# Kernel optimization log

Measured on AMD Instinct MI355X. Metric: run time of the kernel, lower is better.

The kernel has to match this reference:

```python
import jax, jax.numpy as jnp
import numpy as np

N_NODES = 50000
N_EDGES = 800000
D = 128
N_LAYERS = 5  # 1 input + 3 hidden + 1 output MaxAggConv layers


def setup_inputs() -> dict:
    key = jax.random.key(0)
    k1, k2, k3, k4 = jax.random.split(key, 4)
    x = jax.random.normal(k1, (N_NODES, D), dtype=jnp.float32)
    edge_index = jax.random.randint(k2, (2, N_EDGES), 0, N_NODES, dtype=jnp.int64)
    # Linear params per layer (all layers are D->D here): W [out,in], b [out]
    Ws = jax.random.normal(k3, (N_LAYERS, D, D), dtype=jnp.float32) * (1.0 / np.sqrt(D))
    bs = jax.random.normal(k4, (N_LAYERS, D), dtype=jnp.float32) * 0.01
    return {"x": x, "edge_index": edge_index, "Ws": Ws, "bs": bs}


def _max_agg_conv(x, src, dst, W, b, n_nodes):
    # Linear: x @ W^T + b  (nn.Linear convention)
    h = jnp.einsum('nd,od->no', x, W) + b
    # gather per-edge messages x_j (source nodes), scatter-max into targets
    m = jax.ops.segment_max(h[src], dst, num_segments=n_nodes)
    # PyG scatter-max fills nodes with no incoming edges with 0
    return jnp.where(jnp.isneginf(m), 0.0, m)


def reference(x, edge_index, Ws, bs):
    src = edge_index[0]
    dst = edge_index[1]
    n = x.shape[0]
    for i in range(N_LAYERS - 1):
        x = _max_agg_conv(x, src, dst, Ws[i], bs[i], n)
        x = jax.nn.silu(x)
    x = _max_agg_conv(x, src, dst, Ws[N_LAYERS - 1], bs[N_LAYERS - 1], n)
    return x
```

## Files before the change

### kernel.cpp

```cpp
#include <hip/hip_runtime.h>
#include <hip/hip_bf16.h>
#include <hip/hip_fp16.h>
#include <math.h>

#define DF 128
#define NLAYERS 5

typedef __attribute__((ext_vector_type(8))) _Float16 f16x8;
typedef __attribute__((ext_vector_type(4))) _Float16 f16x4;
typedef __attribute__((ext_vector_type(4))) float f32x4;

__device__ inline unsigned pkmax(unsigned a, unsigned b) {
    unsigned d;
    asm("v_pk_max_f16 %0, %1, %2" : "=v"(d) : "v"(a), "v"(b));
    return d;
}
__device__ inline float h2f(unsigned short u) {
    __half_raw r; r.x = u;
    return __half2float(__half(r));
}
__device__ inline float silu(float v) {
    return v * (1.0f / (1.0f + __expf(-v)));
}

__device__ inline void split8f(const float* p, f16x8& hi, f16x8& lo) {
    float4 v0 = *reinterpret_cast<const float4*>(p);
    float4 v1 = *reinterpret_cast<const float4*>(p + 4);
    float f[8] = {v0.x, v0.y, v0.z, v0.w, v1.x, v1.y, v1.z, v1.w};
#pragma unroll
    for (int j = 0; j < 8; ++j) {
        _Float16 a = (_Float16)f[j];
        hi[j] = a;
        lo[j] = (_Float16)(f[j] - (float)a);
    }
}


__global__ __launch_bounds__(256) void zero_kernel(int* __restrict__ p, int n) {
    int i = blockIdx.x * 256 + threadIdx.x;
    if (i < n) p[i] = 0;
}


__global__ __launch_bounds__(256) void prep_kernel(const int* __restrict__ dst,
        int* __restrict__ cnt, unsigned short* __restrict__ rank, int E, int nbE,
        const float* __restrict__ Ws, _Float16* __restrict__ whf,
        _Float16* __restrict__ wlf, int wt4) {
    int b = blockIdx.x;
    int t = threadIdx.x;
    if (b < nbE) {
        int i = b * 256 + t;
        if (i < E) rank[i] = (unsigned short)atomicAdd(&cnt[dst[i]], 1);
    } else {
        int i = (b - nbE) * 256 + t;
        if (i < wt4) {
            float4 v = reinterpret_cast<const float4*>(Ws)[i];
            float f[4] = {v.x, v.y, v.z, v.w};
            f16x4 h, l;
#pragma unroll
            for (int j = 0; j < 4; ++j) {
                _Float16 a = (_Float16)f[j];
                h[j] = a;
                l[j] = (_Float16)(f[j] - (float)a);
            }
            reinterpret_cast<f16x4*>(whf)[i] = h;
            reinterpret_cast<f16x4*>(wlf)[i] = l;
        }
    }
}


__global__ __launch_bounds__(256) void partial_sum_kernel(const int* __restrict__ cnt,
        int* __restrict__ bsum, int n) {
    __shared__ int red[256];
    int t = threadIdx.x;
    int i = blockIdx.x * 256 + t;
    red[t] = (i < n) ? cnt[i] : 0;
    __syncthreads();
    for (int d = 128; d > 0; d >>= 1) {
        if (t < d) red[t] += red[t + d];
        __syncthreads();
    }
    if (t == 0) bsum[blockIdx.x] = red[0];
}

__global__ __launch_bounds__(256) void scan_scatter_kernel(const int* __restrict__ cnt,
        const int* __restrict__ bsum, int* __restrict__ off, int n, int E, int nb) {
    __shared__ int sb[256];
    __shared__ int s[256];
    int t = threadIdx.x;
    int bv = (t < nb) ? bsum[t] : 0;
    sb[t] = bv;
    __syncthreads();
    for (int d = 1; d < 256; d <<= 1) {
        int u = (t >= d) ? sb[t - d] : 0;
        __syncthreads();
        sb[t] += u;
        __syncthreads();
    }
    int base = (blockIdx.x > 0) ? sb[blockIdx.x - 1] : 0;
    int i = blockIdx.x * 256 + t;
    int v = (i < n) ? cnt[i] : 0;
    s[t] = v;
    __syncthreads();
    for (int d = 1; d < 256; d <<= 1) {
        int u = (t >= d) ? s[t - d] : 0;
        __syncthreads();
        s[t] += u;
        __syncthreads();
    }
    int excl = s[t] - v + base;
    if (i < n) off[i] = excl;
    if (blockIdx.x == 0 && t == 0) off[n] = E;
}


__global__ __launch_bounds__(256, 3) void fill_gemm0_kernel(
        const int* __restrict__ src, const int* __restrict__ dst,
        const int* __restrict__ off, const unsigned short* __restrict__ rank,
        unsigned short* __restrict__ csr, int E, int nbE,
        const float* __restrict__ x,
        const _Float16* __restrict__ whf, const _Float16* __restrict__ wlf,
        const float* __restrict__ bias, __half* __restrict__ h, int n) {
    if (blockIdx.x < nbE) {
        int i = blockIdx.x * 256 + threadIdx.x;
        if (i < E) csr[off[dst[i]] + (int)rank[i]] = (unsigned short)src[i];
        return;
    }
    int bid = blockIdx.x - nbE;

    int wave = threadIdx.x >> 6;
    int lane = threadIdx.x & 63;
    int wm = wave >> 1;
    int wn = wave & 1;
    int m0 = bid * 64 + wm * 32;
    int n0 = wn * 64;
    int lr = lane & 15;
    int lk = lane >> 4;

    f32x4 acc[2][4];
#pragma unroll
    for (int mt = 0; mt < 2; ++mt)
#pragma unroll
        for (int nt = 0; nt < 4; ++nt) {
            float bv = bias[n0 + nt * 16 + lr];
            acc[mt][nt] = (f32x4){bv, bv, bv, bv};
        }

    int rowA0 = min(m0 + lr, n - 1);
    int rowA1 = min(m0 + 16 + lr, n - 1);

#pragma unroll
    for (int ks = 0; ks < 4; ++ks) {
        int ko = ks * 32 + lk * 8;
        f16x8 a0h, a0l, a1h, a1l;
        split8f(x + (size_t)rowA0 * DF + ko, a0h, a0l);
        split8f(x + (size_t)rowA1 * DF + ko, a1h, a1l);
#pragma unroll
        for (int nt = 0; nt < 4; ++nt) {
            int ncol = n0 + nt * 16 + lr;
            f16x8 wh = *(const f16x8*)(whf + ncol * DF + ko);
            f16x8 wl = *(const f16x8*)(wlf + ncol * DF + ko);
            acc[0][nt] = __builtin_amdgcn_mfma_f32_16x16x32_f16(a0h, wh, acc[0][nt], 0, 0, 0);
            acc[0][nt] = __builtin_amdgcn_mfma_f32_16x16x32_f16(a0l, wh, acc[0][nt], 0, 0, 0);
            acc[0][nt] = __builtin_amdgcn_mfma_f32_16x16x32_f16(a0h, wl, acc[0][nt], 0, 0, 0);
            acc[1][nt] = __builtin_amdgcn_mfma_f32_16x16x32_f16(a1h, wh, acc[1][nt], 0, 0, 0);
            acc[1][nt] = __builtin_amdgcn_mfma_f32_16x16x32_f16(a1l, wh, acc[1][nt], 0, 0, 0);
            acc[1][nt] = __builtin_amdgcn_mfma_f32_16x16x32_f16(a1h, wl, acc[1][nt], 0, 0, 0);
        }
    }

#pragma unroll
    for (int mt = 0; mt < 2; ++mt) {
        int rbase = m0 + mt * 16 + lk * 4;
#pragma unroll
        for (int j = 0; j < 4; ++j) {
            int r = rbase + j;
            if (r < n) {
#pragma unroll
                for (int nt = 0; nt < 4; ++nt)
                    h[(size_t)r * DF + n0 + nt * 16 + lr] = __float2half(acc[mt][nt][j]);
            }
        }
    }
}


__global__ __launch_bounds__(256, 3) void gemm_f16_kernel(
        const _Float16* __restrict__ xf,
        const _Float16* __restrict__ whf, const _Float16* __restrict__ wlf,
        const float* __restrict__ bias, __half* __restrict__ h, int n) {
    int wave = threadIdx.x >> 6;
    int lane = threadIdx.x & 63;
    int wm = wave >> 1;
    int wn = wave & 1;
    int m0 = blockIdx.x * 64 + wm * 32;
    int n0 = wn * 64;
    int lr = lane & 15;
    int lk = lane >> 4;

    f32x4 acc[2][4];
#pragma unroll
    for (int mt = 0; mt < 2; ++mt)
#pragma unroll
        for (int nt = 0; nt < 4; ++nt) {
            float bv = bias[n0 + nt * 16 + lr];
            acc[mt][nt] = (f32x4){bv, bv, bv, bv};
        }

    int rowA0 = min(m0 + lr, n - 1);
    int rowA1 = min(m0 + 16 + lr, n - 1);

#pragma unroll
    for (int ks = 0; ks < 4; ++ks) {
        int ko = ks * 32 + lk * 8;
        f16x8 a0 = *(const f16x8*)(xf + (size_t)rowA0 * DF + ko);
        f16x8 a1 = *(const f16x8*)(xf + (size_t)rowA1 * DF + ko);
#pragma unroll
        for (int nt = 0; nt < 4; ++nt) {
            int ncol = n0 + nt * 16 + lr;
            f16x8 wh = *(const f16x8*)(whf + ncol * DF + ko);
            f16x8 wl = *(const f16x8*)(wlf + ncol * DF + ko);
            acc[0][nt] = __builtin_amdgcn_mfma_f32_16x16x32_f16(a0, wh, acc[0][nt], 0, 0, 0);
            acc[0][nt] = __builtin_amdgcn_mfma_f32_16x16x32_f16(a0, wl, acc[0][nt], 0, 0, 0);
            acc[1][nt] = __builtin_amdgcn_mfma_f32_16x16x32_f16(a1, wh, acc[1][nt], 0, 0, 0);
            acc[1][nt] = __builtin_amdgcn_mfma_f32_16x16x32_f16(a1, wl, acc[1][nt], 0, 0, 0);
        }
    }

#pragma unroll
    for (int mt = 0; mt < 2; ++mt) {
        int rbase = m0 + mt * 16 + lk * 4;
#pragma unroll
        for (int j = 0; j < 4; ++j) {
            int r = rbase + j;
            if (r < n) {
#pragma unroll
                for (int nt = 0; nt < 4; ++nt)
                    h[(size_t)r * DF + n0 + nt * 16 + lr] = __float2half(acc[mt][nt][j]);
            }
        }
    }
}


__global__ __launch_bounds__(256) void agg_kernel(const __half* __restrict__ hin,
        const int* __restrict__ off, const unsigned short* __restrict__ csr,
        float* __restrict__ out, _Float16* __restrict__ xf, int n, int split) {
    int wid = threadIdx.x >> 6;
    int lane = threadIdx.x & 63;
    int node = blockIdx.x * 4 + wid;
    if (node >= n) return;

    int hf = lane >> 5;
    int l = lane & 31;
    const uint2* h2 = (const uint2*)hin;

    int beg = off[node];
    int end = off[node + 1];

    unsigned m0 = 0xFC00FC00u;
    unsigned m1 = 0xFC00FC00u;

    int e1 = end - 1;
    for (int k = beg; k < end; k += 16) {
        int k0 = k + hf;
        int i0 = min(k0,      e1), i1 = min(k0 + 2,  e1);
        int i2 = min(k0 + 4,  e1), i3 = min(k0 + 6,  e1);
        int i4 = min(k0 + 8,  e1), i5 = min(k0 + 10, e1);
        int i6 = min(k0 + 12, e1), i7 = min(k0 + 14, e1);
        int s0 = csr[i0], s1 = csr[i1], s2 = csr[i2], s3 = csr[i3];
        int s4 = csr[i4], s5 = csr[i5], s6 = csr[i6], s7 = csr[i7];
        uint2 a0 = h2[s0 * 32 + l];
        uint2 a1 = h2[s1 * 32 + l];
        uint2 a2 = h2[s2 * 32 + l];
        uint2 a3 = h2[s3 * 32 + l];
        uint2 a4 = h2[s4 * 32 + l];
        uint2 a5 = h2[s5 * 32 + l];
        uint2 a6 = h2[s6 * 32 + l];
        uint2 a7 = h2[s7 * 32 + l];
        m0 = pkmax(m0, pkmax(pkmax(pkmax(a0.x, a1.x), pkmax(a2.x, a3.x)),
                             pkmax(pkmax(a4.x, a5.x), pkmax(a6.x, a7.x))));
        m1 = pkmax(m1, pkmax(pkmax(pkmax(a0.y, a1.y), pkmax(a2.y, a3.y)),
                             pkmax(pkmax(a4.y, a5.y), pkmax(a6.y, a7.y))));
    }

    m0 = pkmax(m0, (unsigned)__shfl_xor((int)m0, 32));
    m1 = pkmax(m1, (unsigned)__shfl_xor((int)m1, 32));

    if (hf != 0) return;

    float f0 = h2f((unsigned short)(m0 & 0xFFFF));
    float f1 = h2f((unsigned short)(m0 >> 16));
    float f2 = h2f((unsigned short)(m1 & 0xFFFF));
    float f3 = h2f((unsigned short)(m1 >> 16));
    if (beg == end) { f0 = f1 = f2 = f3 = 0.0f; }

    if (split) {
        f0 = silu(f0); f1 = silu(f1); f2 = silu(f2); f3 = silu(f3);
        f16x4 v = { (_Float16)f0, (_Float16)f1, (_Float16)f2, (_Float16)f3 };
        *reinterpret_cast<f16x4*>(xf + (size_t)node * DF + l * 4) = v;
    } else {
        float4 v = make_float4(f0, f1, f2, f3);
        reinterpret_cast<float4*>(out)[node * 32 + l] = v;
    }
}


extern "C" void kernel_launch(void* const* d_in, const int* in_sizes, int n_in,
                              void* d_out, int out_size, void* d_ws, size_t ws_size,
                              hipStream_t stream) {
    const float* x  = (const float*)d_in[0];
    const int*   ei = (const int*)d_in[1];
    const float* Ws = (const float*)d_in[2];
    const float* bs = (const float*)d_in[3];
    float* out = (float*)d_out;

    int N = in_sizes[0] / DF;
    int E = in_sizes[1] / 2;
    const int* src = ei;
    const int* dst = ei + E;

    char* w = (char*)d_ws;
    auto carve = [&](size_t bytes) {
        char* p = w;
        w += (bytes + 255) & ~(size_t)255;
        return p;
    };
    int nb = (N + 255) / 256;
    int*            cnt  = (int*)carve((size_t)(N + 1) * sizeof(int));
    int*            off  = (int*)carve((size_t)(N + 1) * sizeof(int));
    int*            bsum = (int*)carve((size_t)nb * sizeof(int));
    unsigned short* rank = (unsigned short*)carve((size_t)E * sizeof(unsigned short));
    unsigned short* csr  = (unsigned short*)carve((size_t)E * sizeof(unsigned short));
    __half*         h    = (__half*)carve((size_t)N * DF * sizeof(__half));
    _Float16*       xf   = (_Float16*)carve((size_t)N * DF * sizeof(_Float16));
    _Float16*       whf  = (_Float16*)carve((size_t)NLAYERS * DF * DF * sizeof(_Float16));
    _Float16*       wlf  = (_Float16*)carve((size_t)NLAYERS * DF * DF * sizeof(_Float16));

    int nbE = (E + 255) / 256;
    int wt4 = NLAYERS * DF * DF / 4;
    int nbW = (wt4 + 255) / 256;
    int ggrid = (N + 63) / 64;
    int agrid = (N + 3) / 4;

    zero_kernel<<<nb, 256, 0, stream>>>(cnt, N);
    prep_kernel<<<nbE + nbW, 256, 0, stream>>>(dst, cnt, rank, E, nbE, Ws, whf, wlf, wt4);
    partial_sum_kernel<<<nb, 256, 0, stream>>>(cnt, bsum, N);
    scan_scatter_kernel<<<nb, 256, 0, stream>>>(cnt, bsum, off, N, E, nb);

    fill_gemm0_kernel<<<nbE + ggrid, 256, 0, stream>>>(
        src, dst, off, rank, csr, E, nbE, x, whf, wlf, bs, h, N);

    for (int layer = 1; layer < NLAYERS; ++layer) {
        agg_kernel<<<agrid, 256, 0, stream>>>(h, off, csr, out, xf, N, 1);
        const _Float16* whl = whf + (size_t)layer * DF * DF;
        const _Float16* wll = wlf + (size_t)layer * DF * DF;
        const float* bl = bs + (size_t)layer * DF;
        gemm_f16_kernel<<<ggrid, 256, 0, stream>>>(xf, whl, wll, bl, h, N);
    }
    agg_kernel<<<agrid, 256, 0, stream>>>(h, off, csr, out, NULL, N, 0);
}
```

Before: 332.3 us.

## Fuse max-aggregation and SiLU with next layer GEMM via LDS staging

Each hidden layer now runs in one 1024-thread kernel. The kernel gathers neighbour max values for 64 nodes, applies SiLU, stores the result in swizzled LDS and then runs the MFMA GEMM from LDS. This removes the intermediate xf round trip through global memory and one launch per layer, and uses ping-pong h buffers. The gather also changes to 16-byte loads with four edges in flight per lane, where it previously used 8-byte loads with eight. In exchange, the GEMM must wait at a block barrier for the gather to finish, large blocks can lower occupancy, and less memory-level parallelism per lane could slow the gather.

After: 363.7 us. 1.09x slower.

```diff
diff --git a/kernel.cpp b/kernel.cpp
--- a/kernel.cpp
+++ b/kernel.cpp
@@ -186,124 +186,170 @@
 }
 
 
-__global__ __launch_bounds__(256, 3) void gemm_f16_kernel(
-        const _Float16* __restrict__ xf,
+__global__ __launch_bounds__(1024, 2) void fused_layer_kernel(
+        const __half* __restrict__ hin,
+        const int* __restrict__ off, const unsigned short* __restrict__ csr,
         const _Float16* __restrict__ whf, const _Float16* __restrict__ wlf,
-        const float* __restrict__ bias, __half* __restrict__ h, int n) {
+        const float* __restrict__ bias, __half* __restrict__ hout, int n) {
+    __shared__ __align__(16) char xlds[64 * 256];
+
     int wave = threadIdx.x >> 6;
     int lane = threadIdx.x & 63;
-    int wm = wave >> 1;
-    int wn = wave & 1;
-    int m0 = blockIdx.x * 64 + wm * 32;
-    int n0 = wn * 64;
+    int q = lane >> 4;
+    int c = lane & 15;
+    int nodebase = blockIdx.x * 64;
+
+    if (nodebase + 64 > n) {
+        for (int ofs = threadIdx.x * 16; ofs < 64 * 256; ofs += 1024 * 16)
+            *(uint4*)(xlds + ofs) = make_uint4(0, 0, 0, 0);
+        __syncthreads();
+    }
+
+#pragma unroll
+    for (int i = 0; i < 4; ++i) {
+        int r = wave * 4 + i;
+        int node = nodebase + r;
+        if (node < n) {
+            int beg = off[node];
+            int end = off[node + 1];
+            unsigned m0 = 0xFC00FC00u, m1 = m0, m2 = m0, m3 = m0;
+            if (beg < end) {
+                int e1 = end - 1;
+                for (int k = beg; k < end; k += 16) {
+                    int i0 = min(k + q,      e1), i1 = min(k + q + 4,  e1);
+                    int i2 = min(k + q + 8,  e1), i3 = min(k + q + 12, e1);
+                    int s0 = csr[i0], s1 = csr[i1], s2 = csr[i2], s3 = csr[i3];
+                    uint4 a = *(const uint4*)((const char*)hin + ((size_t)s0 << 8) + (c << 4));
+                    uint4 b = *(const uint4*)((const char*)hin + ((size_t)s1 << 8) + (c << 4));
+                    uint4 d = *(const uint4*)((const char*)hin + ((size_t)s2 << 8) + (c << 4));
+                    uint4 e = *(const uint4*)((const char*)hin + ((size_t)s3 << 8) + (c << 4));
+                    m0 = pkmax(m0, pkmax(pkmax(a.x, b.x), pkmax(d.x, e.x)));
+                    m1 = pkmax(m1, pkmax(pkmax(a.y, b.y), pkmax(d.y, e.y)));
+                    m2 = pkmax(m2, pkmax(pkmax(a.z, b.z), pkmax(d.z, e.z)));
+                    m3 = pkmax(m3, pkmax(pkmax(a.w, b.w), pkmax(d.w, e.w)));
+                }
+                m0 = pkmax(m0, (unsigned)__shfl_xor((int)m0, 16));
+                m0 = pkmax(m0, (unsigned)__shfl_xor((int)m0, 32));
+                m1 = pkmax(m1, (unsigned)__shfl_xor((int)m1, 16));
+                m1 = pkmax(m1, (unsigned)__shfl_xor((int)m1, 32));
+                m2 = pkmax(m2, (unsigned)__shfl_xor((int)m2, 16));
+                m2 = pkmax(m2, (unsigned)__shfl_xor((int)m2, 32));
+                m3 = pkmax(m3, (unsigned)__shfl_xor((int)m3, 16));
+                m3 = pkmax(m3, (unsigned)__shfl_xor((int)m3, 32));
+            }
+            if (q == 0) {
+                float f[8];
+                f[0] = h2f((unsigned short)(m0 & 0xFFFF)); f[1] = h2f((unsigned short)(m0 >> 16));
+                f[2] = h2f((unsigned short)(m1 & 0xFFFF)); f[3] = h2f((unsigned short)(m1 >> 16));
+                f[4] = h2f((unsigned short)(m2 & 0xFFFF)); f[5] = h2f((unsigned short)(m2 >> 16));
+                f[6] = h2f((unsigned short)(m3 & 0xFFFF)); f[7] = h2f((unsigned short)(m3 >> 16));
+                f16x8 v;
+#pragma unroll
+                for (int j = 0; j < 8; ++j) {
+                    float t = (beg == end) ? 0.0f : silu(f[j]);
+                    v[j] = (_Float16)t;
+                }
+                int bc = (c << 4) ^ ((r & 7) << 4);
+                *(f16x8*)(xlds + r * 256 + bc) = v;
+            }
+        }
+    }
+    __syncthreads();
+
+    int rt = (wave & 3) * 16;
+    int n0 = (wave >> 2) * 32;
     int lr = lane & 15;
     int lk = lane >> 4;
 
-    f32x4 acc[2][4];
-#pragma unroll
-    for (int mt = 0; mt < 2; ++mt)
-#pragma unroll
-        for (int nt = 0; nt < 4; ++nt) {
-            float bv = bias[n0 + nt * 16 + lr];
-            acc[mt][nt] = (f32x4){bv, bv, bv, bv};
-        }
-
-    int rowA0 = min(m0 + lr, n - 1);
-    int rowA1 = min(m0 + 16 + lr, n - 1);
-
+    f32x4 acc[2];
+#pragma unroll
+    for (int nt = 0; nt < 2; ++nt) {
+        float bv = bias[n0 + nt * 16 + lr];
+        acc[nt] = (f32x4){bv, bv, bv, bv};
+    }
+
+    int ar = rt + lr;
 #pragma unroll
     for (int ks = 0; ks < 4; ++ks) {
+        int bo = ks * 64 + lk * 16;
+        f16x8 a = *(const f16x8*)(xlds + ar * 256 + (bo ^ ((ar & 7) << 4)));
         int ko = ks * 32 + lk * 8;
-        f16x8 a0 = *(const f16x8*)(xf + (size_t)rowA0 * DF + ko);
-        f16x8 a1 = *(const f16x8*)(xf + (size_t)rowA1 * DF + ko);
-#pragma unroll
-        for (int nt = 0; nt < 4; ++nt) {
+#pragma unroll
+        for (int nt = 0; nt < 2; ++nt) {
             int ncol = n0 + nt * 16 + lr;
             f16x8 wh = *(const f16x8*)(whf + ncol * DF + ko);
             f16x8 wl = *(const f16x8*)(wlf + ncol * DF + ko);
-            acc[0][nt] = __builtin_amdgcn_mfma_f32_16x16x32_f16(a0, wh, acc[0][nt], 0, 0, 0);
-            acc[0][nt] = __builtin_amdgcn_mfma_f32_16x16x32_f16(a0, wl, acc[0][nt], 0, 0, 0);
-            acc[1][nt] = __builtin_amdgcn_mfma_f32_16x16x32_f16(a1, wh, acc[1][nt], 0, 0, 0);
-            acc[1][nt] = __builtin_amdgcn_mfma_f32_16x16x32_f16(a1, wl, acc[1][nt], 0, 0, 0);
-        }
-    }
-
-#pragma unroll
-    for (int mt = 0; mt < 2; ++mt) {
-        int rbase = m0 + mt * 16 + lk * 4;
-#pragma unroll
-        for (int j = 0; j < 4; ++j) {
-            int r = rbase + j;
-            if (r < n) {
-#pragma unroll
-                for (int nt = 0; nt < 4; ++nt)
-                    h[(size_t)r * DF + n0 + nt * 16 + lr] = __float2half(acc[mt][nt][j]);
-            }
-        }
-    }
-}
-
-
-__global__ __launch_bounds__(256) void agg_kernel(const __half* __restrict__ hin,
+            acc[nt] = __builtin_amdgcn_mfma_f32_16x16x32_f16(a, wh, acc[nt], 0, 0, 0);
+            acc[nt] = __builtin_amdgcn_mfma_f32_16x16x32_f16(a, wl, acc[nt], 0, 0, 0);
+        }
+    }
+
+#pragma unroll
+    for (int j = 0; j < 4; ++j) {
+        int row = nodebase + rt + lk * 4 + j;
+        if (row < n) {
+#pragma unroll
+            for (int nt = 0; nt < 2; ++nt)
+                hout[(size_t)row * DF + n0 + nt * 16 + lr] = __float2half(acc[nt][j]);
+        }
+    }
+}
+
+
+__global__ __launch_bounds__(256) void agg_final_kernel(const __half* __restrict__ hin,
         const int* __restrict__ off, const unsigned short* __restrict__ csr,
-        float* __restrict__ out, _Float16* __restrict__ xf, int n, int split) {
+        float* __restrict__ out, int n) {
     int wid = threadIdx.x >> 6;
     int lane = threadIdx.x & 63;
     int node = blockIdx.x * 4 + wid;
     if (node >= n) return;
 
-    int hf = lane >> 5;
-    int l = lane & 31;
-    const uint2* h2 = (const uint2*)hin;
+    int q = lane >> 4;
+    int c = lane & 15;
 
     int beg = off[node];
     int end = off[node + 1];
 
-    unsigned m0 = 0xFC00FC00u;
-    unsigned m1 = 0xFC00FC00u;
-
-    int e1 = end - 1;
-    for (int k = beg; k < end; k += 16) {
-        int k0 = k + hf;
-        int i0 = min(k0,      e1), i1 = min(k0 + 2,  e1);
-        int i2 = min(k0 + 4,  e1), i3 = min(k0 + 6,  e1);
-        int i4 = min(k0 + 8,  e1), i5 = min(k0 + 10, e1);
-        int i6 = min(k0 + 12, e1), i7 = min(k0 + 14, e1);
-        int s0 = csr[i0], s1 = csr[i1], s2 = csr[i2], s3 = csr[i3];
-        int s4 = csr[i4], s5 = csr[i5], s6 = csr[i6], s7 = csr[i7];
-        uint2 a0 = h2[s0 * 32 + l];
-        uint2 a1 = h2[s1 * 32 + l];
-        uint2 a2 = h2[s2 * 32 + l];
-        uint2 a3 = h2[s3 * 32 + l];
-        uint2 a4 = h2[s4 * 32 + l];
-        uint2 a5 = h2[s5 * 32 + l];
-        uint2 a6 = h2[s6 * 32 + l];
-        uint2 a7 = h2[s7 * 32 + l];
-        m0 = pkmax(m0, pkmax(pkmax(pkmax(a0.x, a1.x), pkmax(a2.x, a3.x)),
-                             pkmax(pkmax(a4.x, a5.x), pkmax(a6.x, a7.x))));
-        m1 = pkmax(m1, pkmax(pkmax(pkmax(a0.y, a1.y), pkmax(a2.y, a3.y)),
-                             pkmax(pkmax(a4.y, a5.y), pkmax(a6.y, a7.y))));
-    }
-
-    m0 = pkmax(m0, (unsigned)__shfl_xor((int)m0, 32));
-    m1 = pkmax(m1, (unsigned)__shfl_xor((int)m1, 32));
-
-    if (hf != 0) return;
-
-    float f0 = h2f((unsigned short)(m0 & 0xFFFF));
-    float f1 = h2f((unsigned short)(m0 >> 16));
-    float f2 = h2f((unsigned short)(m1 & 0xFFFF));
-    float f3 = h2f((unsigned short)(m1 >> 16));
-    if (beg == end) { f0 = f1 = f2 = f3 = 0.0f; }
-
-    if (split) {
-        f0 = silu(f0); f1 = silu(f1); f2 = silu(f2); f3 = silu(f3);
-        f16x4 v = { (_Float16)f0, (_Float16)f1, (_Float16)f2, (_Float16)f3 };
-        *reinterpret_cast<f16x4*>(xf + (size_t)node * DF + l * 4) = v;
-    } else {
-        float4 v = make_float4(f0, f1, f2, f3);
-        reinterpret_cast<float4*>(out)[node * 32 + l] = v;
-    }
+    unsigned m0 = 0xFC00FC00u, m1 = m0, m2 = m0, m3 = m0;
+    if (beg < end) {
+        int e1 = end - 1;
+        for (int k = beg; k < end; k += 16) {
+            int i0 = min(k + q,      e1), i1 = min(k + q + 4,  e1);
+            int i2 = min(k + q + 8,  e1), i3 = min(k + q + 12, e1);
+            int s0 = csr[i0], s1 = csr[i1], s2 = csr[i2], s3 = csr[i3];
+            uint4 a = *(const uint4*)((const char*)hin + ((size_t)s0 << 8) + (c << 4));
+            uint4 b = *(const uint4*)((const char*)hin + ((size_t)s1 << 8) + (c << 4));
+            uint4 d = *(const uint4*)((const char*)hin + ((size_t)s2 << 8) + (c << 4));
+            uint4 e = *(const uint4*)((const char*)hin + ((size_t)s3 << 8) + (c << 4));
+            m0 = pkmax(m0, pkmax(pkmax(a.x, b.x), pkmax(d.x, e.x)));
+            m1 = pkmax(m1, pkmax(pkmax(a.y, b.y), pkmax(d.y, e.y)));
+            m2 = pkmax(m2, pkmax(pkmax(a.z, b.z), pkmax(d.z, e.z)));
+            m3 = pkmax(m3, pkmax(pkmax(a.w, b.w), pkmax(d.w, e.w)));
+        }
+        m0 = pkmax(m0, (unsigned)__shfl_xor((int)m0, 16));
+        m0 = pkmax(m0, (unsigned)__shfl_xor((int)m0, 32));
+        m1 = pkmax(m1, (unsigned)__shfl_xor((int)m1, 16));
+        m1 = pkmax(m1, (unsigned)__shfl_xor((int)m1, 32));
+        m2 = pkmax(m2, (unsigned)__shfl_xor((int)m2, 16));
+        m2 = pkmax(m2, (unsigned)__shfl_xor((int)m2, 32));
+        m3 = pkmax(m3, (unsigned)__shfl_xor((int)m3, 16));
+        m3 = pkmax(m3, (unsigned)__shfl_xor((int)m3, 32));
+    }
+
+    if (q != 0) return;
+
+    float f[8];
+    f[0] = h2f((unsigned short)(m0 & 0xFFFF)); f[1] = h2f((unsigned short)(m0 >> 16));
+    f[2] = h2f((unsigned short)(m1 & 0xFFFF)); f[3] = h2f((unsigned short)(m1 >> 16));
+    f[4] = h2f((unsigned short)(m2 & 0xFFFF)); f[5] = h2f((unsigned short)(m2 >> 16));
+    f[6] = h2f((unsigned short)(m3 & 0xFFFF)); f[7] = h2f((unsigned short)(m3 >> 16));
+    if (beg == end) {
+#pragma unroll
+        for (int j = 0; j < 8; ++j) f[j] = 0.0f;
+    }
+    float4* o = (float4*)(out + (size_t)node * DF + c * 8);
+    o[0] = make_float4(f[0], f[1], f[2], f[3]);
+    o[1] = make_float4(f[4], f[5], f[6], f[7]);
 }
 
 
@@ -333,8 +379,8 @@
     int*            bsum = (int*)carve((size_t)nb * sizeof(int));
     unsigned short* rank = (unsigned short*)carve((size_t)E * sizeof(unsigned short));
     unsigned short* csr  = (unsigned short*)carve((size_t)E * sizeof(unsigned short));
-    __half*         h    = (__half*)carve((size_t)N * DF * sizeof(__half));
-    _Float16*       xf   = (_Float16*)carve((size_t)N * DF * sizeof(_Float16));
+    __half*         hA   = (__half*)carve((size_t)N * DF * sizeof(__half));
+    __half*         hB   = (__half*)carve((size_t)N * DF * sizeof(__half));
     _Float16*       whf  = (_Float16*)carve((size_t)NLAYERS * DF * DF * sizeof(_Float16));
     _Float16*       wlf  = (_Float16*)carve((size_t)NLAYERS * DF * DF * sizeof(_Float16));
 
@@ -350,14 +396,18 @@
     scan_scatter_kernel<<<nb, 256, 0, stream>>>(cnt, bsum, off, N, E, nb);
 
     fill_gemm0_kernel<<<nbE + ggrid, 256, 0, stream>>>(
-        src, dst, off, rank, csr, E, nbE, x, whf, wlf, bs, h, N);
-
+        src, dst, off, rank, csr, E, nbE, x, whf, wlf, bs, hA, N);
+
+    __half* hin = hA;
+    __half* hout = hB;
     for (int layer = 1; layer < NLAYERS; ++layer) {
-        agg_kernel<<<agrid, 256, 0, stream>>>(h, off, csr, out, xf, N, 1);
         const _Float16* whl = whf + (size_t)layer * DF * DF;
         const _Float16* wll = wlf + (size_t)layer * DF * DF;
         const float* bl = bs + (size_t)layer * DF;
-        gemm_f16_kernel<<<ggrid, 256, 0, stream>>>(xf, whl, wll, bl, h, N);
-    }
-    agg_kernel<<<agrid, 256, 0, stream>>>(h, off, csr, out, NULL, N, 0);
-}
+        fused_layer_kernel<<<ggrid, 1024, 0, stream>>>(
+            hin, off, csr, whl, wll, bl, hout, N);
+        __half* t = hin; hin = hout; hout = t;
+    }
+
+    agg_final_kernel<<<agrid, 256, 0, stream>>>(hin, off, csr, out, N);
+}
```

## Gather neighbor rows with 16-byte loads and wave-shuffled CSR indices

Applied to the files above, without the earlier changes.

Restructures the max-aggregation gather so each wavefront loads up to 64 CSR neighbor indices cooperatively with one coalesced load, then broadcasts them via shuffles. Each quarter-wave of 16 lanes reads a full 256-byte fp16 row with 16-byte vector loads, so four edges are handled per load instruction group instead of two edges with 8-byte loads. The reduction becomes a two-step cross-quarter shuffle. Fewer redundant index loads and wider gathers aim to cut memory instruction overhead; the price is extra shuffles, and low-degree nodes leave lanes idle.

After: 324.6 us, median of 2. 2.3% less time.

```diff
diff --git a/kernel.cpp b/kernel.cpp
--- a/kernel.cpp
+++ b/kernel.cpp
@@ -252,57 +252,66 @@
     int node = blockIdx.x * 4 + wid;
     if (node >= n) return;
 
-    int hf = lane >> 5;
-    int l = lane & 31;
-    const uint2* h2 = (const uint2*)hin;
+    int q = lane >> 4;
+    int c = lane & 15;
 
     int beg = off[node];
     int end = off[node + 1];
 
-    unsigned m0 = 0xFC00FC00u;
-    unsigned m1 = 0xFC00FC00u;
-
-    int e1 = end - 1;
-    for (int k = beg; k < end; k += 16) {
-        int k0 = k + hf;
-        int i0 = min(k0,      e1), i1 = min(k0 + 2,  e1);
-        int i2 = min(k0 + 4,  e1), i3 = min(k0 + 6,  e1);
-        int i4 = min(k0 + 8,  e1), i5 = min(k0 + 10, e1);
-        int i6 = min(k0 + 12, e1), i7 = min(k0 + 14, e1);
-        int s0 = csr[i0], s1 = csr[i1], s2 = csr[i2], s3 = csr[i3];
-        int s4 = csr[i4], s5 = csr[i5], s6 = csr[i6], s7 = csr[i7];
-        uint2 a0 = h2[s0 * 32 + l];
-        uint2 a1 = h2[s1 * 32 + l];
-        uint2 a2 = h2[s2 * 32 + l];
-        uint2 a3 = h2[s3 * 32 + l];
-        uint2 a4 = h2[s4 * 32 + l];
-        uint2 a5 = h2[s5 * 32 + l];
-        uint2 a6 = h2[s6 * 32 + l];
-        uint2 a7 = h2[s7 * 32 + l];
-        m0 = pkmax(m0, pkmax(pkmax(pkmax(a0.x, a1.x), pkmax(a2.x, a3.x)),
-                             pkmax(pkmax(a4.x, a5.x), pkmax(a6.x, a7.x))));
-        m1 = pkmax(m1, pkmax(pkmax(pkmax(a0.y, a1.y), pkmax(a2.y, a3.y)),
-                             pkmax(pkmax(a4.y, a5.y), pkmax(a6.y, a7.y))));
-    }
-
-    m0 = pkmax(m0, (unsigned)__shfl_xor((int)m0, 32));
-    m1 = pkmax(m1, (unsigned)__shfl_xor((int)m1, 32));
-
-    if (hf != 0) return;
-
-    float f0 = h2f((unsigned short)(m0 & 0xFFFF));
-    float f1 = h2f((unsigned short)(m0 >> 16));
-    float f2 = h2f((unsigned short)(m1 & 0xFFFF));
-    float f3 = h2f((unsigned short)(m1 >> 16));
-    if (beg == end) { f0 = f1 = f2 = f3 = 0.0f; }
+    unsigned m0 = 0xFC00FC00u, m1 = m0, m2 = m0, m3 = m0;
+
+    if (beg < end) {
+        int e1 = end - 1;
+        int deg = end - beg;
+        for (int base = 0; base < deg; base += 64) {
+            int myid = csr[min(beg + base + lane, e1)];
+            int lim = min(deg - base, 64);
+            for (int t = 0; t < lim; t += 16) {
+                int i0 = __shfl(myid, t + q);
+                int i1 = __shfl(myid, t + q + 4);
+                int i2 = __shfl(myid, t + q + 8);
+                int i3 = __shfl(myid, t + q + 12);
+                uint4 a = *(const uint4*)((const char*)hin + ((size_t)i0 << 8) + (c << 4));
+                uint4 b = *(const uint4*)((const char*)hin + ((size_t)i1 << 8) + (c << 4));
+                uint4 d = *(const uint4*)((const char*)hin + ((size_t)i2 << 8) + (c << 4));
+                uint4 e = *(const uint4*)((const char*)hin + ((size_t)i3 << 8) + (c << 4));
+                m0 = pkmax(m0, pkmax(pkmax(a.x, b.x), pkmax(d.x, e.x)));
+                m1 = pkmax(m1, pkmax(pkmax(a.y, b.y), pkmax(d.y, e.y)));
+                m2 = pkmax(m2, pkmax(pkmax(a.z, b.z), pkmax(d.z, e.z)));
+                m3 = pkmax(m3, pkmax(pkmax(a.w, b.w), pkmax(d.w, e.w)));
+            }
+        }
+        m0 = pkmax(m0, (unsigned)__shfl_xor((int)m0, 16));
+        m0 = pkmax(m0, (unsigned)__shfl_xor((int)m0, 32));
+        m1 = pkmax(m1, (unsigned)__shfl_xor((int)m1, 16));
+        m1 = pkmax(m1, (unsigned)__shfl_xor((int)m1, 32));
+        m2 = pkmax(m2, (unsigned)__shfl_xor((int)m2, 16));
+        m2 = pkmax(m2, (unsigned)__shfl_xor((int)m2, 32));
+        m3 = pkmax(m3, (unsigned)__shfl_xor((int)m3, 16));
+        m3 = pkmax(m3, (unsigned)__shfl_xor((int)m3, 32));
+    }
+
+    if (q != 0) return;
+
+    float f[8];
+    f[0] = h2f((unsigned short)(m0 & 0xFFFF)); f[1] = h2f((unsigned short)(m0 >> 16));
+    f[2] = h2f((unsigned short)(m1 & 0xFFFF)); f[3] = h2f((unsigned short)(m1 >> 16));
+    f[4] = h2f((unsigned short)(m2 & 0xFFFF)); f[5] = h2f((unsigned short)(m2 >> 16));
+    f[6] = h2f((unsigned short)(m3 & 0xFFFF)); f[7] = h2f((unsigned short)(m3 >> 16));
+    if (beg == end) {
+#pragma unroll
+        for (int j = 0; j < 8; ++j) f[j] = 0.0f;
+    }
 
     if (split) {
-        f0 = silu(f0); f1 = silu(f1); f2 = silu(f2); f3 = silu(f3);
-        f16x4 v = { (_Float16)f0, (_Float16)f1, (_Float16)f2, (_Float16)f3 };
-        *reinterpret_cast<f16x4*>(xf + (size_t)node * DF + l * 4) = v;
+        f16x8 v;
+#pragma unroll
+        for (int j = 0; j < 8; ++j) v[j] = (_Float16)silu(f[j]);
+        *reinterpret_cast<f16x8*>(xf + (size_t)node * DF + c * 8) = v;
     } else {
-        float4 v = make_float4(f0, f1, f2, f3);
-        reinterpret_cast<float4*>(out)[node * 32 + l] = v;
+        float4* o = (float4*)(out + (size_t)node * DF + c * 8);
+        o[0] = make_float4(f[0], f[1], f[2], f[3]);
+        o[1] = make_float4(f[4], f[5], f[6], f[7]);
     }
 }
 
```
